# Optimization experiments

Hardware: AMD Instinct MI355X
Metric: run time of the kernel (lower is better)

Reference implementation:

```python
import jax, jax.numpy as jnp
import numpy as np

H = 512   # hidden_size
L = 20    # num_labels
B, S = 32, 256


def _uniform(key, shape, k):
    return jax.random.uniform(key, shape, minval=-k, maxval=k, dtype=jnp.float32)


def setup_inputs() -> dict:
    key = jax.random.key(0)
    ks = iter(jax.random.split(key, 40))
    k = 1.0 / np.sqrt(H)
    inp = {
        "inputs": jax.random.normal(next(ks), (B, S, H), dtype=jnp.float32),
        "labels": jax.random.randint(next(ks), (B, S), 0, L),
        "mask": jnp.ones((B, S), dtype=jnp.int32),
    }
    for layer, din in ((0, H), (1, 2 * H)):
        for d in ("f", "b"):
            inp[f"w_ih_l{layer}{d}"] = _uniform(next(ks), (4 * H, din), k)
            inp[f"w_hh_l{layer}{d}"] = _uniform(next(ks), (4 * H, H), k)
            inp[f"b_ih_l{layer}{d}"] = _uniform(next(ks), (4 * H,), k)
            inp[f"b_hh_l{layer}{d}"] = _uniform(next(ks), (4 * H,), k)
    kf = 1.0 / np.sqrt(2 * H)
    inp["fc_w"] = _uniform(next(ks), (L, 2 * H), kf)
    inp["fc_b"] = _uniform(next(ks), (L,), kf)
    inp["trans_m"] = jax.random.normal(next(ks), (L, L), dtype=jnp.float32) * 0.1
    inp["start_scores"] = jax.random.normal(next(ks), (L,), dtype=jnp.float32) * 0.1
    inp["end_scores"] = jax.random.normal(next(ks), (L,), dtype=jnp.float32) * 0.1
    return inp


def _lstm_dir(x, wih, whh, bih, bhh, reverse):
    # x: [S, B, Din] -> hs: [S, B, H] (outputs in original time order)
    _, b, _ = x.shape
    hh = whh.shape[1]
    xw = jnp.einsum('sbd,gd->sbg', x, wih) + bih + bhh  # precompute input projections

    def step(carry, xt):
        h, c = carry
        g = xt + h @ whh.T  # [B, 4H]
        i, f, gg, o = jnp.split(g, 4, axis=-1)  # pytorch gate order i,f,g,o
        c = jax.nn.sigmoid(f) * c + jax.nn.sigmoid(i) * jnp.tanh(gg)
        h = jax.nn.sigmoid(o) * jnp.tanh(c)
        return (h, c), h

    init = (jnp.zeros((b, hh), x.dtype), jnp.zeros((b, hh), x.dtype))
    _, hs = jax.lax.scan(step, init, xw, reverse=reverse)
    return hs


def _crf_loss(logits, tags, maskf, trans, start, end):
    # logits [S,B,L], tags [S,B], maskf [S,B] float. Returns per-sample NLL [B].
    s, b, n = logits.shape
    # --- normalizer (forward algorithm) ---
    alpha0 = logits[0] + start  # [B, n]

    def step(alpha, inp):
        emit, m = inp  # emit [B,n], m [B]
        tmp = alpha[:, :, None] + trans[None, :, :] + emit[:, None, :]  # [B, from, to]
        new = jax.nn.logsumexp(tmp, axis=1)
        alpha = jnp.where(m[:, None] > 0, new, alpha)
        return alpha, None

    alpha, _ = jax.lax.scan(step, alpha0, (logits[1:], maskf[1:]))
    norm = jax.nn.logsumexp(alpha + end, axis=1)  # [B]
    # --- gold path score ---
    emit = jnp.take_along_axis(logits, tags[:, :, None], axis=2)[:, :, 0] * maskf  # [S,B]
    trans_sc = trans[tags[:-1], tags[1:]] * maskf[1:]  # [S-1,B]
    last_idx = maskf.sum(0).astype(jnp.int32) - 1  # [B]
    last_tags = tags[last_idx, jnp.arange(b)]
    gold = emit.sum(0) + trans_sc.sum(0) + start[tags[0]] + end[last_tags]
    return norm - gold


def reference(inputs, labels, mask,
              w_ih_l0f, w_hh_l0f, b_ih_l0f, b_hh_l0f,
              w_ih_l0b, w_hh_l0b, b_ih_l0b, b_hh_l0b,
              w_ih_l1f, w_hh_l1f, b_ih_l1f, b_hh_l1f,
              w_ih_l1b, w_hh_l1b, b_ih_l1b, b_hh_l1b,
              fc_w, fc_b, trans_m, start_scores, end_scores):
    x = jnp.transpose(inputs, (1, 0, 2))  # [S,B,H]
    h0 = jnp.concatenate([
        _lstm_dir(x, w_ih_l0f, w_hh_l0f, b_ih_l0f, b_hh_l0f, False),
        _lstm_dir(x, w_ih_l0b, w_hh_l0b, b_ih_l0b, b_hh_l0b, True),
    ], axis=-1)  # [S,B,2H]
    h1 = jnp.concatenate([
        _lstm_dir(h0, w_ih_l1f, w_hh_l1f, b_ih_l1f, b_hh_l1f, False),
        _lstm_dir(h0, w_ih_l1b, w_hh_l1b, b_ih_l1b, b_hh_l1b, True),
    ], axis=-1)  # [S,B,2H]
    logits = h1 @ fc_w.T + fc_b  # [S,B,L]
    tags = labels.T  # [S,B]
    maskf = mask.T.astype(logits.dtype)
    loss = _crf_loss(logits, tags, maskf, trans_m, start_scores, end_scores)
    return loss.mean()
```

## Files before the change

### kernel.cpp

```cpp
#include <hip/hip_runtime.h>

#define Sx 256
#define Bx 32
#define Hx 512
#define Gx 2048
#define Lx 20
#define Rx 8192

typedef __attribute__((ext_vector_type(8))) short short8;
typedef __attribute__((ext_vector_type(4))) float f32x4;
typedef __attribute__((ext_vector_type(16))) float f32x16;

__device__ __forceinline__ unsigned short f2bf(float f) {
  union { float f; unsigned u; } v; v.f = f;
  unsigned u = v.u;
  return (unsigned short)((u + 0x7fffu + ((u >> 16) & 1u)) >> 16);
}
__device__ __forceinline__ float bf2f(unsigned short h) {
  union { unsigned u; float f; } v; v.u = ((unsigned)h) << 16;
  return v.f;
}
__device__ __forceinline__ float bfh(unsigned long long x, int r) {
  return bf2f((unsigned short)((x >> (16 * r)) & 0xffffull));
}
__device__ __forceinline__ float sigmf(float x) { return 1.0f / (1.0f + expf(-x)); }

__device__ __forceinline__ float fsigm(float x) {
  return __builtin_amdgcn_rcpf(1.0f + __builtin_amdgcn_exp2f(-1.44269504f * x));
}
__device__ __forceinline__ float ftanh(float x) {
  return __builtin_fmaf(-2.0f,
      __builtin_amdgcn_rcpf(1.0f + __builtin_amdgcn_exp2f(2.88539008f * x)), 1.0f);
}


__global__ void k_pack_x(const float* __restrict__ x, unsigned short* __restrict__ xbf) {
  int tid = blockIdx.x * 256 + threadIdx.x;
  int h = tid & (Hx - 1);
  int r = tid >> 9;
  int b = r & 31;
  int t = r >> 5;
  xbf[tid] = f2bf(x[(b * Sx + t) * Hx + h]);
}

__global__ void k_cast(const float* __restrict__ s, unsigned short* __restrict__ d, int n) {
  int i = blockIdx.x * 256 + threadIdx.x;
  if (i < n) d[i] = f2bf(s[i]);
}

__global__ void k_add2(const float* __restrict__ a, const float* __restrict__ b,
                       float* __restrict__ o, int n) {
  int i = blockIdx.x * 256 + threadIdx.x;
  if (i < n) o[i] = a[i] + b[i];
}

__global__ void k_repack(const unsigned short* __restrict__ hT, unsigned short* __restrict__ rows) {
  int tid = blockIdx.x * 256 + threadIdx.x;
  int b = tid & 31;
  int kt = (tid >> 5) & 63;
  int t = (tid >> 11) & 255;
  int dir = tid >> 19;
  short8 v = *(const short8*)&hT[(size_t)tid * 8];
  *(short8*)&rows[((size_t)(t * 32 + b)) * 1024 + dir * 512 + kt * 8] = v;
}

__global__ __launch_bounds__(256) void k_gemm(
    const unsigned short* __restrict__ A,
    const unsigned short* __restrict__ Bw,
    const float* __restrict__ bias,
    unsigned short* __restrict__ C,
    int M, int N, int K)
{
  const int bn = blockIdx.x, bm = blockIdx.y;
  const int tid = threadIdx.x;
  const int w = tid >> 6, lane = tid & 63;
  const int wr = w >> 1, wc = w & 1;
  const int lo = lane & 15, qd = lane >> 4;

  __shared__ unsigned short As[128 * 72];
  __shared__ unsigned short Bs[128 * 72];

  f32x4 acc[4][4] = {};

  const int ktn = K >> 6;
  for (int kt = 0; kt < ktn; ++kt) {
    __syncthreads();
#pragma unroll
    for (int p = 0; p < 4; ++p) {
      int c = tid + (p << 8);
      int row = c >> 3, kc = c & 7;
      *(short8*)&As[row * 72 + kc * 8] =
          *(const short8*)&A[(size_t)(bm * 128 + row) * K + kt * 64 + kc * 8];
      *(short8*)&Bs[row * 72 + kc * 8] =
          *(const short8*)&Bw[(size_t)(bn * 128 + row) * K + kt * 64 + kc * 8];
    }
    __syncthreads();
#pragma unroll
    for (int kk = 0; kk < 2; ++kk) {
      short8 af[4], bfr[4];
#pragma unroll
      for (int mi = 0; mi < 4; ++mi)
        af[mi] = *(const short8*)&As[(wr * 64 + mi * 16 + lo) * 72 + kk * 32 + qd * 8];
#pragma unroll
      for (int ni = 0; ni < 4; ++ni)
        bfr[ni] = *(const short8*)&Bs[(wc * 64 + ni * 16 + lo) * 72 + kk * 32 + qd * 8];
#pragma unroll
      for (int mi = 0; mi < 4; ++mi)
#pragma unroll
        for (int ni = 0; ni < 4; ++ni)
          acc[mi][ni] = __builtin_amdgcn_mfma_f32_16x16x32_bf16(af[mi], bfr[ni], acc[mi][ni], 0, 0, 0);
    }
  }
#pragma unroll
  for (int mi = 0; mi < 4; ++mi) {
#pragma unroll
    for (int ni = 0; ni < 4; ++ni) {
      int n = bn * 128 + wc * 64 + ni * 16 + lo;
      float bv = bias[n];
      int wsb = (n >> 4) & 31, cg = n >> 9, jl = n & 15;
      size_t base = (size_t)wsb * (Rx * 64) + (size_t)cg * 16 + jl;
#pragma unroll
      for (int r = 0; r < 4; ++r) {
        int m = bm * 128 + wr * 64 + mi * 16 + qd * 4 + r;
        C[base + (size_t)m * 64] = f2bf(acc[mi][ni][r] + bv);
      }
    }
  }
}

__global__ __launch_bounds__(256, 1) void k_lstm(
    const unsigned short* __restrict__ xwF,
    const unsigned short* __restrict__ xwB,
    const unsigned short* __restrict__ whF,
    const unsigned short* __restrict__ whB,
    unsigned short* __restrict__ hT,
    unsigned int* __restrict__ flags,
    unsigned int* __restrict__ done)
{
  const int wg = blockIdx.x;
  const int tid = threadIdx.x;

  __shared__ unsigned short Ws[64 * 512];

  if (wg >= 64) {
    asm volatile("s_setprio 0");
    float a = 1.0f + (float)tid, bm = 1.0000001f, cm = 1.0e-7f;
    for (;;) {
#pragma unroll 8
      for (int i = 0; i < 512; ++i) a = __builtin_fmaf(a, bm, cm);
      if (__hip_atomic_load(done, __ATOMIC_RELAXED, __HIP_MEMORY_SCOPE_AGENT) >= 64u) break;
    }
    if (a == 123.456789f) ((volatile float*)hT)[0] = a;
    return;
  }

  asm volatile("s_setprio 3");
  const int dir = wg >> 5;
  const int vs = wg & 31;
  const int j0 = vs * 16;
  const unsigned short* xw = (dir ? xwB : xwF) + (size_t)vs * (Rx * 64);
  const unsigned short* wh = dir ? whB : whF;
  unsigned short* hTd = hT + (size_t)dir * (Sx * 16384);
  unsigned int* fl = flags + dir * 32 * 32;

  {
    const int l6 = tid & 63;
#pragma unroll
    for (int i = 0; i < 16; ++i) {
      int rr = (tid >> 6) * 16 + i;
      int g = ((rr >> 4) << 9) + j0 + (rr & 15);
      int pc = l6 ^ (rr & 7);
      *(short8*)&Ws[rr * 512 + pc * 8] = *(const short8*)&wh[(size_t)g * Hx + l6 * 8];
    }
  }
  __syncthreads();
  if (tid >= 64) return;

  const int lane = tid;
  const int bn = lane & 31;
  const int q  = lane >> 5;

  float cst[2][4] = {};

  for (int s = 0; s < Sx; ++s) {
    const int t = dir ? (Sx - 1 - s) : s;

    const unsigned short* xwt = xw + ((size_t)t * 32 + bn) * 64 + q * 4;
    unsigned long long xg[4][2];
#pragma unroll
    for (int c = 0; c < 4; ++c)
#pragma unroll
      for (int jg = 0; jg < 2; ++jg)
        xg[c][jg] = *(const unsigned long long*)(xwt + c * 16 + jg * 8);
    __asm__ __volatile__("" ::: "memory");

    f32x16 acc0, acc1;

    if (s > 0) {
      const unsigned tgt = (unsigned)s;
      const int tp = dir ? (t + 1) : (t - 1);
      const unsigned short* hb = hTd + (size_t)tp * 16384 + lane * 8;

      short8 hreg[32];
      for (;;) {
        unsigned v = __hip_atomic_load(fl + (lane & 31) * 32,
                                       __ATOMIC_RELAXED, __HIP_MEMORY_SCOPE_AGENT);
#pragma unroll
        for (int ks = 0; ks < 32; ++ks)
          hreg[ks] = *(const short8*)(hb + ks * 512);
#pragma unroll
        for (int ks = 0; ks < 32; ++ks)
          asm volatile("" :: "v"(hreg[ks]));
        if (__all((int)(v >= tgt))) break;
        __asm__ __volatile__("" ::: "memory");
      }
      __builtin_amdgcn_sched_barrier(0);

      f32x16 a0 = {}, a1 = {}, b0 = {}, b1 = {};
#pragma unroll
      for (int ks = 0; ks < 32; ks += 2) {
        int lc0 = ks * 2 + q, lc1 = (ks + 1) * 2 + q;
        int pc0 = lc0 ^ (bn & 7), pc1 = lc1 ^ (bn & 7);
        short8 af00 = *(const short8*)&Ws[bn * 512 + pc0 * 8];
        short8 af10 = *(const short8*)&Ws[(32 + bn) * 512 + pc0 * 8];
        short8 af01 = *(const short8*)&Ws[bn * 512 + pc1 * 8];
        short8 af11 = *(const short8*)&Ws[(32 + bn) * 512 + pc1 * 8];
        a0 = __builtin_amdgcn_mfma_f32_32x32x16_bf16(af00, hreg[ks],     a0, 0, 0, 0);
        a1 = __builtin_amdgcn_mfma_f32_32x32x16_bf16(af10, hreg[ks],     a1, 0, 0, 0);
        b0 = __builtin_amdgcn_mfma_f32_32x32x16_bf16(af01, hreg[ks + 1], b0, 0, 0, 0);
        b1 = __builtin_amdgcn_mfma_f32_32x32x16_bf16(af11, hreg[ks + 1], b1, 0, 0, 0);
      }
      acc0 = a0 + b0;
      acc1 = a1 + b1;
    } else {
      acc0 = (f32x16){};
      acc1 = (f32x16){};
    }

#pragma unroll
    for (int jg = 0; jg < 2; ++jg) {
      unsigned long long hv = 0;
#pragma unroll
      for (int r = 0; r < 4; ++r) {
        float iv = acc0[jg * 4 + r]     + bfh(xg[0][jg], r);
        float fv = acc0[8 + jg * 4 + r] + bfh(xg[1][jg], r);
        float gv = acc1[jg * 4 + r]     + bfh(xg[2][jg], r);
        float ov = acc1[8 + jg * 4 + r] + bfh(xg[3][jg], r);
        float ct = fsigm(fv) * cst[jg][r] + fsigm(iv) * ftanh(gv);
        cst[jg][r] = ct;
        float hvf = fsigm(ov) * ftanh(ct);
        hv |= (unsigned long long)f2bf(hvf) << (16 * r);
      }
      unsigned short* hw = hTd + (size_t)t * 16384 + ((size_t)(vs * 2 + jg) * 32 + bn) * 8 + q * 4;
      __hip_atomic_store((unsigned long long*)hw, hv,
                         __ATOMIC_RELAXED, __HIP_MEMORY_SCOPE_AGENT);
    }

    __asm__ __volatile__("s_waitcnt vmcnt(0)" ::: "memory");
    if (lane == 0)
      __hip_atomic_store(fl + vs * 32, (unsigned)(s + 1),
                         __ATOMIC_RELAXED, __HIP_MEMORY_SCOPE_AGENT);
  }

  if (lane == 0)
    __hip_atomic_fetch_add(done, 1u, __ATOMIC_RELAXED, __HIP_MEMORY_SCOPE_AGENT);
}

__global__ __launch_bounds__(256) void k_fc(
    const unsigned short* __restrict__ h1T,
    const float* __restrict__ fcw,
    const float* __restrict__ fcb,
    float* __restrict__ logits)
{
  int row = blockIdx.x;
  int t = row >> 5, b = row & 31;
  int l = threadIdx.x & 31;
  int sl = threadIdx.x >> 5;
  __shared__ float red[8][32];
  float p = 0.f;
  if (l < Lx) {
#pragma unroll 4
    for (int kt = sl * 16; kt < sl * 16 + 16; ++kt) {
      int k = kt * 8;
      int dir = k >> 9, kk = k & 511;
      const unsigned short* hp = h1T + (size_t)dir * (Sx * 16384) + (size_t)t * 16384
                                 + ((size_t)(kk >> 3) * 32 + b) * 8;
      const float* wr = fcw + l * 1024 + k;
#pragma unroll
      for (int e = 0; e < 8; ++e) p += bf2f(hp[e]) * wr[e];
    }
  }
  red[sl][l] = p;
  __syncthreads();
  if (threadIdx.x < Lx) {
    float s = fcb[threadIdx.x];
#pragma unroll
    for (int i = 0; i < 8; ++i) s += red[i][threadIdx.x];
    logits[(size_t)row * Lx + threadIdx.x] = s;
  }
}

__global__ __launch_bounds__(64) void k_crf(
    const float* __restrict__ logits,
    const int* __restrict__ labels,
    const int* __restrict__ mask,
    const float* __restrict__ trans,
    const float* __restrict__ startv,
    const float* __restrict__ endv,
    float* __restrict__ out)
{
  int b = blockIdx.x;
  int tid = threadIdx.x;
  __shared__ float tr[Lx * Lx];
  __shared__ float al[2][Lx];
  __shared__ float norm_s;
  for (int i = tid; i < Lx * Lx; i += 64) tr[i] = trans[i];
  if (tid < Lx) al[0][tid] = logits[b * Lx + tid] + startv[tid];
  __syncthreads();
  int cur = 0;
  for (int t = 1; t < Sx; ++t) {
    if (tid < Lx) {
      int to = tid;
      float v[Lx];
      float mx = -1e30f;
#pragma unroll
      for (int f = 0; f < Lx; ++f) { v[f] = al[cur][f] + tr[f * Lx + to]; mx = fmaxf(mx, v[f]); }
      float sum = 0.f;
#pragma unroll
      for (int f = 0; f < Lx; ++f) sum += expf(v[f] - mx);
      float nv = mx + logf(sum) + logits[((size_t)t * Bx + b) * Lx + to];
      int m = mask[b * Sx + t];
      al[1 - cur][to] = (m > 0) ? nv : al[cur][to];
    }
    __syncthreads();
    cur ^= 1;
  }
  if (tid == 0) {
    float mx = -1e30f;
    for (int l = 0; l < Lx; ++l) mx = fmaxf(mx, al[cur][l] + endv[l]);
    float s = 0.f;
    for (int l = 0; l < Lx; ++l) s += expf(al[cur][l] + endv[l] - mx);
    norm_s = mx + logf(s);
  }
  __syncthreads();
  const int* lab = labels + b * Sx;
  const int* msk = mask + b * Sx;
  float part = 0.f;
  int msum = 0;
  for (int t = tid; t < Sx; t += 64) {
    int m = msk[t];
    int tg = lab[t];
    if (m > 0) {
      part += logits[((size_t)t * Bx + b) * Lx + tg];
      if (t >= 1) part += tr[lab[t - 1] * Lx + tg];
      msum++;
    }
  }
#pragma unroll
  for (int o = 32; o > 0; o >>= 1) {
    part += __shfl_down(part, o, 64);
    msum += __shfl_down(msum, o, 64);
  }
  if (tid == 0) {
    float gold = part + startv[lab[0]] + endv[lab[msum - 1]];
    atomicAdd(out, (norm_s - gold) * (1.0f / 32.0f));
  }
}


extern "C" void kernel_launch(void* const* d_in, const int* in_sizes, int n_in,
                              void* d_out, int out_size, void* d_ws, size_t ws_size,
                              hipStream_t stream)
{
  const float* x      = (const float*)d_in[0];
  const int* labels   = (const int*)d_in[1];
  const int* mask     = (const int*)d_in[2];
  const float* wih0f  = (const float*)d_in[3];
  const float* whh0f  = (const float*)d_in[4];
  const float* bih0f  = (const float*)d_in[5];
  const float* bhh0f  = (const float*)d_in[6];
  const float* wih0b  = (const float*)d_in[7];
  const float* whh0b  = (const float*)d_in[8];
  const float* bih0b  = (const float*)d_in[9];
  const float* bhh0b  = (const float*)d_in[10];
  const float* wih1f  = (const float*)d_in[11];
  const float* whh1f  = (const float*)d_in[12];
  const float* bih1f  = (const float*)d_in[13];
  const float* bhh1f  = (const float*)d_in[14];
  const float* wih1b  = (const float*)d_in[15];
  const float* whh1b  = (const float*)d_in[16];
  const float* bih1b  = (const float*)d_in[17];
  const float* bhh1b  = (const float*)d_in[18];
  const float* fcw    = (const float*)d_in[19];
  const float* fcb    = (const float*)d_in[20];
  const float* transm = (const float*)d_in[21];
  const float* startv = (const float*)d_in[22];
  const float* endv   = (const float*)d_in[23];

  char* p = (char*)d_ws;
  auto alloc = [&](size_t bytes) -> char* {
    char* r = p;
    p += (bytes + 255) & ~((size_t)255);
    return r;
  };

  unsigned short* x_bf    = (unsigned short*)alloc((size_t)Rx * Hx * 2);
  unsigned short* wih0f_b = (unsigned short*)alloc((size_t)Gx * Hx * 2);
  unsigned short* wih0b_b = (unsigned short*)alloc((size_t)Gx * Hx * 2);
  unsigned short* whh0f_b = (unsigned short*)alloc((size_t)Gx * Hx * 2);
  unsigned short* whh0b_b = (unsigned short*)alloc((size_t)Gx * Hx * 2);
  unsigned short* wih1f_b = (unsigned short*)alloc((size_t)Gx * 1024 * 2);
  unsigned short* wih1b_b = (unsigned short*)alloc((size_t)Gx * 1024 * 2);
  unsigned short* whh1f_b = (unsigned short*)alloc((size_t)Gx * Hx * 2);
  unsigned short* whh1b_b = (unsigned short*)alloc((size_t)Gx * Hx * 2);
  float* bias0f = (float*)alloc(Gx * 4);
  float* bias0b = (float*)alloc(Gx * 4);
  float* bias1f = (float*)alloc(Gx * 4);
  float* bias1b = (float*)alloc(Gx * 4);
  unsigned short* xw_f = (unsigned short*)alloc((size_t)Rx * Gx * 2);
  unsigned short* xw_b = (unsigned short*)alloc((size_t)Rx * Gx * 2);
  unsigned short* h0T  = (unsigned short*)alloc((size_t)2 * Sx * 16384 * 2);
  unsigned short* h1T  = (unsigned short*)alloc((size_t)2 * Sx * 16384 * 2);
  unsigned short* h0rows = (unsigned short*)alloc((size_t)Rx * 1024 * 2);
  float* logits = (float*)alloc((size_t)Rx * Lx * 4);
  unsigned int* flagsA = (unsigned int*)alloc(2 * 32 * 32 * 4);
  unsigned int* flagsB = (unsigned int*)alloc(2 * 32 * 32 * 4);
  unsigned int* doneA  = (unsigned int*)alloc(256);
  unsigned int* doneB  = (unsigned int*)alloc(256);

  if ((size_t)(p - (char*)d_ws) > ws_size) return;

  hipMemsetAsync(flagsA, 0, 2 * 32 * 32 * 4, stream);
  hipMemsetAsync(flagsB, 0, 2 * 32 * 32 * 4, stream);
  hipMemsetAsync(doneA, 0, 256, stream);
  hipMemsetAsync(doneB, 0, 256, stream);

  k_pack_x<<<(Rx * Hx) / 256, 256, 0, stream>>>(x, x_bf);
  k_cast<<<(Gx * Hx) / 256, 256, 0, stream>>>(wih0f, wih0f_b, Gx * Hx);
  k_cast<<<(Gx * Hx) / 256, 256, 0, stream>>>(wih0b, wih0b_b, Gx * Hx);
  k_cast<<<(Gx * Hx) / 256, 256, 0, stream>>>(whh0f, whh0f_b, Gx * Hx);
  k_cast<<<(Gx * Hx) / 256, 256, 0, stream>>>(whh0b, whh0b_b, Gx * Hx);
  k_cast<<<(Gx * 1024) / 256, 256, 0, stream>>>(wih1f, wih1f_b, Gx * 1024);
  k_cast<<<(Gx * 1024) / 256, 256, 0, stream>>>(wih1b, wih1b_b, Gx * 1024);
  k_cast<<<(Gx * Hx) / 256, 256, 0, stream>>>(whh1f, whh1f_b, Gx * Hx);
  k_cast<<<(Gx * Hx) / 256, 256, 0, stream>>>(whh1b, whh1b_b, Gx * Hx);
  k_add2<<<Gx / 256, 256, 0, stream>>>(bih0f, bhh0f, bias0f, Gx);
  k_add2<<<Gx / 256, 256, 0, stream>>>(bih0b, bhh0b, bias0b, Gx);
  k_add2<<<Gx / 256, 256, 0, stream>>>(bih1f, bhh1f, bias1f, Gx);
  k_add2<<<Gx / 256, 256, 0, stream>>>(bih1b, bhh1b, bias1b, Gx);

  k_gemm<<<dim3(Gx / 128, Rx / 128), 256, 0, stream>>>(x_bf, wih0f_b, bias0f, xw_f, Rx, Gx, Hx);
  k_gemm<<<dim3(Gx / 128, Rx / 128), 256, 0, stream>>>(x_bf, wih0b_b, bias0b, xw_b, Rx, Gx, Hx);
  k_lstm<<<256, 256, 0, stream>>>(xw_f, xw_b, whh0f_b, whh0b_b, h0T, flagsA, doneA);

  k_repack<<<4096, 256, 0, stream>>>(h0T, h0rows);

  k_gemm<<<dim3(Gx / 128, Rx / 128), 256, 0, stream>>>(h0rows, wih1f_b, bias1f, xw_f, Rx, Gx, 1024);
  k_gemm<<<dim3(Gx / 128, Rx / 128), 256, 0, stream>>>(h0rows, wih1b_b, bias1b, xw_b, Rx, Gx, 1024);
  k_lstm<<<256, 256, 0, stream>>>(xw_f, xw_b, whh1f_b, whh1b_b, h1T, flagsB, doneB);

  k_fc<<<Rx, 256, 0, stream>>>(h1T, fcw, fcb, logits);
  hipMemsetAsync(d_out, 0, 4, stream);
  k_crf<<<Bx, 64, 0, stream>>>(logits, labels, mask, transm, startv, endv, (float*)d_out);
}
```

Baseline: 2.636 ms.

## Restructure LSTM flag spin-wait, vectorize FC loads, prefetch and fast-math CRF

```diff
diff --git a/kernel.cpp b/kernel.cpp
--- a/kernel.cpp
+++ b/kernel.cpp
@@ -32,6 +32,8 @@
   return __builtin_fmaf(-2.0f,
       __builtin_amdgcn_rcpf(1.0f + __builtin_amdgcn_exp2f(2.88539008f * x)), 1.0f);
 }
+#define L2E 1.44269504088896f
+#define LN2 0.69314718055995f
 
 
 __global__ void k_pack_x(const float* __restrict__ x, unsigned short* __restrict__ xbf) {
@@ -202,17 +204,28 @@
       const unsigned short* hb = hTd + (size_t)tp * 16384 + lane * 8;
 
       short8 hreg[32];
-      for (;;) {
-        unsigned v = __hip_atomic_load(fl + (lane & 31) * 32,
-                                       __ATOMIC_RELAXED, __HIP_MEMORY_SCOPE_AGENT);
+      unsigned v0 = __hip_atomic_load(fl + (lane & 31) * 32,
+                                      __ATOMIC_RELAXED, __HIP_MEMORY_SCOPE_AGENT);
+#pragma unroll
+      for (int ks = 0; ks < 32; ++ks)
+        hreg[ks] = *(const short8*)(hb + ks * 512);
+#pragma unroll
+      for (int ks = 0; ks < 32; ++ks)
+        asm volatile("" :: "v"(hreg[ks]));
+      if (!__all((int)(v0 >= tgt))) {
+        unsigned v;
+        do {
+          __asm__ __volatile__("" ::: "memory");
+          v = __hip_atomic_load(fl + (lane & 31) * 32,
+                                __ATOMIC_RELAXED, __HIP_MEMORY_SCOPE_AGENT);
+        } while (!__all((int)(v >= tgt)));
+        __asm__ __volatile__("" ::: "memory");
 #pragma unroll
         for (int ks = 0; ks < 32; ++ks)
           hreg[ks] = *(const short8*)(hb + ks * 512);
 #pragma unroll
         for (int ks = 0; ks < 32; ++ks)
           asm volatile("" :: "v"(hreg[ks]));
-        if (__all((int)(v >= tgt))) break;
-        __asm__ __volatile__("" ::: "memory");
       }
       __builtin_amdgcn_sched_barrier(0);
 
@@ -285,9 +298,14 @@
       int dir = k >> 9, kk = k & 511;
       const unsigned short* hp = h1T + (size_t)dir * (Sx * 16384) + (size_t)t * 16384
                                  + ((size_t)(kk >> 3) * 32 + b) * 8;
+      short8 hv = *(const short8*)hp;
       const float* wr = fcw + l * 1024 + k;
-#pragma unroll
-      for (int e = 0; e < 8; ++e) p += bf2f(hp[e]) * wr[e];
+      f32x4 w0 = *(const f32x4*)wr;
+      f32x4 w1 = *(const f32x4*)(wr + 4);
+      p += bf2f((unsigned short)hv[0]) * w0[0] + bf2f((unsigned short)hv[1]) * w0[1]
+         + bf2f((unsigned short)hv[2]) * w0[2] + bf2f((unsigned short)hv[3]) * w0[3]
+         + bf2f((unsigned short)hv[4]) * w1[0] + bf2f((unsigned short)hv[5]) * w1[1]
+         + bf2f((unsigned short)hv[6]) * w1[2] + bf2f((unsigned short)hv[7]) * w1[3];
     }
   }
   red[sl][l] = p;
@@ -318,7 +336,15 @@
   if (tid < Lx) al[0][tid] = logits[b * Lx + tid] + startv[tid];
   __syncthreads();
   int cur = 0;
+  float em = (tid < Lx) ? logits[((size_t)1 * Bx + b) * Lx + tid] : 0.f;
+  int m = mask[b * Sx + 1];
   for (int t = 1; t < Sx; ++t) {
+    float em_next = 0.f;
+    int m_next = 0;
+    if (t + 1 < Sx) {
+      if (tid < Lx) em_next = logits[((size_t)(t + 1) * Bx + b) * Lx + tid];
+      m_next = mask[b * Sx + t + 1];
+    }
     if (tid < Lx) {
       int to = tid;
       float v[Lx];
@@ -327,20 +353,21 @@
       for (int f = 0; f < Lx; ++f) { v[f] = al[cur][f] + tr[f * Lx + to]; mx = fmaxf(mx, v[f]); }
       float sum = 0.f;
 #pragma unroll
-      for (int f = 0; f < Lx; ++f) sum += expf(v[f] - mx);
-      float nv = mx + logf(sum) + logits[((size_t)t * Bx + b) * Lx + to];
-      int m = mask[b * Sx + t];
+      for (int f = 0; f < Lx; ++f) sum += __builtin_amdgcn_exp2f((v[f] - mx) * L2E);
+      float nv = mx + LN2 * __builtin_amdgcn_logf(sum) + em;
       al[1 - cur][to] = (m > 0) ? nv : al[cur][to];
     }
     __syncthreads();
     cur ^= 1;
+    em = em_next;
+    m = m_next;
   }
   if (tid == 0) {
     float mx = -1e30f;
     for (int l = 0; l < Lx; ++l) mx = fmaxf(mx, al[cur][l] + endv[l]);
     float s = 0.f;
-    for (int l = 0; l < Lx; ++l) s += expf(al[cur][l] + endv[l] - mx);
-    norm_s = mx + logf(s);
+    for (int l = 0; l < Lx; ++l) s += __builtin_amdgcn_exp2f((al[cur][l] + endv[l] - mx) * L2E);
+    norm_s = mx + LN2 * __builtin_amdgcn_logf(s);
   }
   __syncthreads();
   const int* lab = labels + b * Sx;
@@ -348,9 +375,9 @@
   float part = 0.f;
   int msum = 0;
   for (int t = tid; t < Sx; t += 64) {
-    int m = msk[t];
+    int mm = msk[t];
     int tg = lab[t];
-    if (m > 0) {
+    if (mm > 0) {
       part += logits[((size_t)t * Bx + b) * Lx + tg];
       if (t >= 1) part += tr[lab[t - 1] * Lx + tg];
       msum++;
```

Result: no change. 2.613 ms (-0.9%).
